# Kernel tuning notes

Hardware: AMD Instinct MI355X
Metric: run time of the kernel (lower is better)

## Reference

```python
import jax, jax.numpy as jnp
import numpy as np

B, SQ, SK, D, H, DFF = 4, 1024, 1024, 1024, 16, 4096
DEPTH = D // H
EPS = 1e-6


def setup_inputs() -> dict:
    key = jax.random.key(0)
    ks = jax.random.split(key, 32)
    s = 0.02
    inp = {
        "x": jax.random.normal(ks[0], (B, SQ, D), jnp.float32),
        "enc_output": jax.random.normal(ks[1], (B, SK, D), jnp.float32),
        # causal look-ahead mask: 1 where attention is disallowed
        "look_ahead_mask": (1.0 - jnp.tril(jnp.ones((SQ, SQ), jnp.float32)))[None, None],
        "padding_mask": jnp.zeros((B, 1, 1, SK), jnp.float32),
    }
    names = ["wq1", "wk1", "wv1", "wo1", "wq2", "wk2", "wv2", "wo2"]
    for i, n in enumerate(names):
        inp[n] = jax.random.normal(ks[2 + i], (D, D), jnp.float32) * s
        inp["b" + n[1:]] = jnp.zeros((D,), jnp.float32)
    inp["w_ffn1"] = jax.random.normal(ks[12], (D, DFF), jnp.float32) * s
    inp["b_ffn1"] = jnp.zeros((DFF,), jnp.float32)
    inp["w_ffn2"] = jax.random.normal(ks[13], (DFF, D), jnp.float32) * s
    inp["b_ffn2"] = jnp.zeros((D,), jnp.float32)
    for i in (1, 2, 3):
        inp[f"gamma{i}"] = jnp.ones((D,), jnp.float32)
        inp[f"beta{i}"] = jnp.zeros((D,), jnp.float32)
    return inp


def _layernorm(x, gamma, beta):
    mu = jnp.mean(x, axis=-1, keepdims=True)
    var = jnp.var(x, axis=-1, keepdims=True)
    return (x - mu) * jax.lax.rsqrt(var + EPS) * gamma + beta


def _split_heads(x):
    b, s, _ = x.shape
    return x.reshape(b, s, H, DEPTH).transpose(0, 2, 1, 3)  # (B,H,S,depth)


def _mha(v_in, k_in, q_in, mask, wq, bq, wk, bk, wv, bv, wo, bo):
    q = _split_heads(q_in @ wq + bq)
    k = _split_heads(k_in @ wk + bk)
    v = _split_heads(v_in @ wv + bv)
    logits = jnp.einsum("bhqd,bhkd->bhqk", q, k) / jnp.sqrt(jnp.float32(DEPTH))
    if mask is not None:
        logits = logits + mask * -1e9
    attn = jax.nn.softmax(logits, axis=-1)
    out = jnp.einsum("bhqk,bhkd->bhqd", attn, v)
    out = out.transpose(0, 2, 1, 3).reshape(q_in.shape[0], -1, D)
    return out @ wo + bo, attn


def reference(x, enc_output, look_ahead_mask, padding_mask,
              wq1, bq1, wk1, bk1, wv1, bv1, wo1, bo1,
              wq2, bq2, wk2, bk2, wv2, bv2, wo2, bo2,
              w_ffn1, b_ffn1, w_ffn2, b_ffn2,
              gamma1, beta1, gamma2, beta2, gamma3, beta3):
    attn1, aw1 = _mha(x, x, x, look_ahead_mask,
                      wq1, bq1, wk1, bk1, wv1, bv1, wo1, bo1)
    out1 = _layernorm(attn1 + x, gamma1, beta1)
    attn2, aw2 = _mha(enc_output, enc_output, out1, padding_mask,
                      wq2, bq2, wk2, bk2, wv2, bv2, wo2, bo2)
    out2 = _layernorm(attn2 + out1, gamma2, beta2)
    ffn = jax.nn.relu(out2 @ w_ffn1 + b_ffn1) @ w_ffn2 + b_ffn2
    out3 = _layernorm(ffn + out2, gamma3, beta3)
    return out3, aw1, aw2
```

## Files before the change

### kernel.cpp

```cpp
#include <hip/hip_runtime.h>

#define NB 4
#define SEQ 1024
#define DM 1024
#define NH 16
#define DEP 64
#define DFFN 4096

typedef __attribute__((ext_vector_type(8))) short short8;
typedef __attribute__((ext_vector_type(4))) float f32x4;
typedef __attribute__((ext_vector_type(4))) unsigned short us4;

__device__ __forceinline__ unsigned short f2bf(float f) {
    union { float f; unsigned int u; } v; v.f = f;
    unsigned int u = v.u;
    return (unsigned short)((u + 0x7FFFu + ((u >> 16) & 1u)) >> 16);
}

__device__ __forceinline__ void gload16(const void* g, void* l) {
    __builtin_amdgcn_global_load_lds((const __attribute__((address_space(1))) unsigned int*)g,
                                     (__attribute__((address_space(3))) unsigned int*)l, 16, 0, 0);
}

__global__ __launch_bounds__(256) void cast2_kernel(const float* __restrict__ a,
                                                    const float* __restrict__ b,
                                                    unsigned short* __restrict__ oa,
                                                    unsigned short* __restrict__ ob, int n4) {
    int i = blockIdx.x * 256 + threadIdx.x;
    const float* in = blockIdx.y ? b : a;
    unsigned short* out = blockIdx.y ? ob : oa;
    if (i < n4) {
        f32x4 f = __builtin_nontemporal_load((const f32x4*)in + i);
        us4 u;
        u[0] = f2bf(f[0]); u[1] = f2bf(f[1]); u[2] = f2bf(f[2]); u[3] = f2bf(f[3]);
        ((us4*)out)[i] = u;
    }
}

struct P10 { const float* p[10]; };
__global__ __launch_bounds__(256) void castTall_kernel(P10 s,
                                                       unsigned short* __restrict__ wsq,
                                                       unsigned short* __restrict__ wf1t,
                                                       unsigned short* __restrict__ wf2t) {
    __shared__ float tile[64][65];
    const int tid = blockIdx.x, t = threadIdx.x;
    const float* in; unsigned short* out; int R, C, r0, c0;
    if (tid < 2048) {
        int wi = tid >> 8, t2 = tid & 255;
        in = s.p[wi]; out = wsq + (size_t)wi * DM * DM; R = DM; C = DM;
        r0 = (t2 >> 4) * 64; c0 = (t2 & 15) * 64;
    } else if (tid < 3072) {
        int t2 = tid - 2048;
        in = s.p[8]; out = wf1t; R = DM; C = DFFN;
        r0 = (t2 >> 6) * 64; c0 = (t2 & 63) * 64;
    } else {
        int t2 = tid - 3072;
        in = s.p[9]; out = wf2t; R = DFFN; C = DM;
        r0 = (t2 >> 4) * 64; c0 = (t2 & 15) * 64;
    }
#pragma unroll
    for (int p = 0; p < 4; ++p) {
        int r = p * 16 + (t >> 4), c = (t & 15) * 4;
        f32x4 f = __builtin_nontemporal_load((const f32x4*)(in + (size_t)(r0 + r) * C + c0 + c));
        tile[r][c] = f[0]; tile[r][c + 1] = f[1]; tile[r][c + 2] = f[2]; tile[r][c + 3] = f[3];
    }
    __syncthreads();
#pragma unroll
    for (int p = 0; p < 4; ++p) {
        int n = p * 16 + (t >> 4), k = (t & 15) * 4;
        us4 u;
#pragma unroll
        for (int j = 0; j < 4; ++j) u[j] = f2bf(tile[k + j][n]);
        *(us4*)(out + (size_t)(c0 + n) * R + r0 + k) = u;
    }
}

__global__ __launch_bounds__(256) void biaspack_kernel(const float* __restrict__ bq1,
                                                       const float* __restrict__ bk1,
                                                       const float* __restrict__ bv1,
                                                       const float* __restrict__ bk2,
                                                       const float* __restrict__ bv2,
                                                       float* __restrict__ bqkv1,
                                                       float* __restrict__ bkv2) {
    int i = blockIdx.x * 256 + threadIdx.x;
    if (i < 1024) bqkv1[i] = bq1[i];
    else if (i < 2048) bqkv1[i] = bk1[i - 1024];
    else if (i < 3072) bqkv1[i] = bv1[i - 2048];
    else if (i < 4096) bkv2[i - 3072] = bk2[i - 3072];
    else if (i < 5120) bkv2[i - 3072] = bv2[i - 4096];
}

template <int BM, int BN, int BK, int KSPLIT, int RELU, int WB, int WF, int WVT>
__global__ __launch_bounds__(256) void gemm_kernel(const unsigned short* __restrict__ A,
                                                   const unsigned short* __restrict__ Wt,
                                                   const float* __restrict__ bias,
                                                   unsigned short* __restrict__ Cb,
                                                   float* __restrict__ Cf,
                                                   float* __restrict__ Cf2,
                                                   unsigned short* __restrict__ Vt,
                                                   int vstart,
                                                   int M, int N, int K) {
    constexpr int AM = BM / 32;
    constexpr int KS = BK / 32;
    constexpr int LPR = BK / 8;
    constexpr int RPI = 64 / LPR;
    constexpr int AR = (BM / 4) / RPI;
    constexpr int BR = (BN / 4) / RPI;
    constexpr int NLD = AR + BR;
    __shared__ unsigned short As[3][BM * BK];
    __shared__ unsigned short Bs[3][BN * BK];
    const int t = threadIdx.x;
    const int lane = t & 63, w = t >> 6;
    const int nwg = gridDim.x * gridDim.y;
    const int rawid = blockIdx.y * gridDim.x + blockIdx.x;
    const int swz = (rawid & 7) * (nwg >> 3) + (rawid >> 3);
    const int m0 = (swz / gridDim.x) * BM, n0 = (swz % gridDim.x) * BN;
    const int wm = (w >> 1) * (BM / 2), wn = (w & 1) * (BN / 2);
    const int lr = lane & 15, g = lane >> 4, kb = g * 8;
    const int srow = lane / LPR;
    const int sslotl = lane % LPR;
    const int sswz = (BK == 64) ? (sslotl ^ srow) : sslotl;
    const int scol = sswz * 8;
    const int kofs = (KSPLIT == 2 && blockIdx.z) ? K / 2 : 0;
    const int Keff = (KSPLIT == 2) ? K / 2 : K;
    const int nk = Keff / BK;

    f32x4 acc[AM][4];
#pragma unroll
    for (int a = 0; a < AM; ++a)
#pragma unroll
        for (int b = 0; b < 4; ++b)
#pragma unroll
            for (int j = 0; j < 4; ++j) acc[a][b][j] = 0.f;

    auto STAGE = [&](int buf, int kt) {
#pragma unroll
        for (int ia = 0; ia < AR; ++ia) {
            int rb = w * (BM / 4) + ia * RPI;
            gload16(A + (size_t)(m0 + rb + srow) * K + kt + scol, &As[buf][rb * BK]);
        }
#pragma unroll
        for (int ib = 0; ib < BR; ++ib) {
            int rb = w * (BN / 4) + ib * RPI;
            gload16(Wt + (size_t)(n0 + rb + srow) * K + kt + scol, &Bs[buf][rb * BK]);
        }
    };

    STAGE(0, kofs);
    if (nk > 1) STAGE(1, kofs + BK);
    int sb = 2, cb = 0;
    for (int i = 0; i < nk; ++i) {
        if (i + 2 < nk) {
            STAGE(sb, kofs + (i + 2) * BK);
            if (++sb == 3) sb = 0;
            asm volatile("s_waitcnt vmcnt(%0)" :: "n"(2 * NLD) : "memory");
        } else if (i + 1 < nk) {
            asm volatile("s_waitcnt vmcnt(%0)" :: "n"(NLD) : "memory");
        } else {
            asm volatile("s_waitcnt vmcnt(0)" ::: "memory");
        }
        __builtin_amdgcn_s_barrier();

        short8 af[AM][KS], bfr[4][KS];
#pragma unroll
        for (int ii = 0; ii < AM; ++ii)
#pragma unroll
            for (int ks = 0; ks < KS; ++ks) {
                int ofs = (BK == 64) ? (((ks * 4 + g) ^ (lr & 7)) << 3) : (ks * 32 + kb);
                af[ii][ks] = *(const short8*)&As[cb][(wm + ii * 16 + lr) * BK + ofs];
            }
#pragma unroll
        for (int ii = 0; ii < 4; ++ii)
#pragma unroll
            for (int ks = 0; ks < KS; ++ks) {
                int ofs = (BK == 64) ? (((ks * 4 + g) ^ (lr & 7)) << 3) : (ks * 32 + kb);
                bfr[ii][ks] = *(const short8*)&Bs[cb][(wn + ii * 16 + lr) * BK + ofs];
            }
        __builtin_amdgcn_s_setprio(1);
#pragma unroll
        for (int ks = 0; ks < KS; ++ks)
#pragma unroll
            for (int am = 0; am < AM; ++am)
#pragma unroll
                for (int bn = 0; bn < 4; ++bn)
                    acc[am][bn] = __builtin_amdgcn_mfma_f32_16x16x32_bf16(af[am][ks], bfr[bn][ks], acc[am][bn], 0, 0, 0);
        __builtin_amdgcn_s_setprio(0);
        if (++cb == 3) cb = 0;
        __builtin_amdgcn_s_barrier();
    }

    float* cfo = (KSPLIT == 2 && blockIdx.z) ? Cf2 : Cf;
    const bool addb = bias && (KSPLIT == 1 || blockIdx.z == 0);
#pragma unroll
    for (int am = 0; am < AM; ++am) {
#pragma unroll
        for (int bn = 0; bn < 4; ++bn) {
            int col = n0 + wn + bn * 16 + lr;
            float bv = addb ? bias[col] : 0.f;
            int rowb = m0 + wm + am * 16 + g * 4;
            float vv[4];
#pragma unroll
            for (int i = 0; i < 4; ++i) {
                float v = acc[am][bn][i] + bv;
                if (RELU) v = v > 0.f ? v : 0.f;
                vv[i] = v;
                if (WF) cfo[(size_t)(rowb + i) * N + col] = v;
                if (WB) Cb[(size_t)(rowb + i) * N + col] = f2bf(v);
            }
            if (WVT && col >= vstart) {
                int h = (col - vstart) >> 6, dep = (col - vstart) & 63;
                int b = rowb >> 10, kpos = rowb & 1023;
                us4 u;
#pragma unroll
                for (int i = 0; i < 4; ++i) u[i] = f2bf(vv[i]);
                *(us4*)(Vt + ((size_t)(b * NH + h) * DEP + dep) * SEQ + kpos) = u;
            }
        }
    }
}

template <int CAUSAL>
__global__ __launch_bounds__(256, 2) void attn_kernel(const unsigned short* __restrict__ Q, int ldq,
                                                      const unsigned short* __restrict__ Kp, int ldk,
                                                      const unsigned short* __restrict__ Vt,
                                                      const float* __restrict__ pad,
                                                      float* __restrict__ aw,
                                                      unsigned short* __restrict__ ctx) {
    __shared__ unsigned short Ks[3][128 * 64];
    __shared__ unsigned short Pch[32 * 128];
    __shared__ float redm[4][32];
    __shared__ float reds[4][32];
    const int t = threadIdx.x, lane = t & 63, w = t >> 6;
    const int lr = lane & 15, g = lane >> 4;
    const int id = blockIdx.x;
    const int bh = (id & 7) + ((id >> 8) << 3);
    const int qt = (id >> 3) & 31;
    const int q0 = qt * 32;
    const int b = bh >> 4, h = bh & 15;
    const size_t qbase = (size_t)b * SEQ * ldq + (size_t)h * DEP;
    const size_t kbase = (size_t)b * SEQ * ldk + (size_t)h * DEP;
    const int cmax = CAUSAL ? (q0 >> 7) + 1 : 8;

    const int srow = lane >> 3;
    const int sslot = (lane & 7) ^ srow;

    short8 aq[2][2];
#pragma unroll
    for (int p = 0; p < 2; ++p)
#pragma unroll
        for (int ks = 0; ks < 2; ++ks)
            aq[p][ks] = *(const short8*)(Q + qbase + (size_t)(q0 + p * 16 + lr) * ldq + ks * 32 + g * 8);

    f32x4 acc[2][8][2];
#pragma unroll
    for (int p = 0; p < 2; ++p)
#pragma unroll
        for (int c = 0; c < 8; ++c)
#pragma unroll
            for (int bn = 0; bn < 2; ++bn)
#pragma unroll
                for (int j = 0; j < 4; ++j) acc[p][c][bn][j] = 0.f;

#define STAGE_K(BUF, CH)                                                                   \
    {                                                                                      \
        _Pragma("unroll") for (int i_ = 0; i_ < 4; ++i_) {                                 \
            int rb_ = w * 32 + i_ * 8;                                                     \
            gload16(Kp + kbase + (size_t)((CH) * 128 + rb_ + srow) * ldk + sslot * 8,      \
                    &Ks[BUF][rb_ * 64]);                                                   \
        }                                                                                  \
    }

    STAGE_K(0, 0);
    if (1 < cmax) STAGE_K(1, 1);
#pragma unroll
    for (int c = 0; c < 8; ++c) {
        if (c < cmax) {
            if (c + 2 < cmax) {
                STAGE_K((c + 2) % 3, c + 2);
                asm volatile("s_waitcnt vmcnt(8)" ::: "memory");
            } else if (c + 1 < cmax) {
                asm volatile("s_waitcnt vmcnt(4)" ::: "memory");
            } else {
                asm volatile("s_waitcnt vmcnt(0)" ::: "memory");
            }
            __builtin_amdgcn_s_setprio(1);
#pragma unroll
            for (int ks = 0; ks < 2; ++ks)
#pragma unroll
                for (int bn = 0; bn < 2; ++bn) {
                    int row = w * 32 + bn * 16 + lr;
                    short8 bk = *(const short8*)((const char*)&Ks[c % 3][0] + row * 128 +
                                                 ((ks * 64 + g * 16) ^ ((lr & 7) << 4)));
                    acc[0][c][bn] = __builtin_amdgcn_mfma_f32_16x16x32_bf16(bk, aq[0][ks], acc[0][c][bn], 0, 0, 0);
                    acc[1][c][bn] = __builtin_amdgcn_mfma_f32_16x16x32_bf16(bk, aq[1][ks], acc[1][c][bn], 0, 0, 0);
                }
            __builtin_amdgcn_s_setprio(0);
        }
    }
#undef STAGE_K

    float mrow[2] = {-1e30f, -1e30f};
#pragma unroll
    for (int c = 0; c < 8; ++c) {
        if (c < cmax) {
#pragma unroll
            for (int bn = 0; bn < 2; ++bn) {
                int k4 = c * 128 + w * 32 + bn * 16 + g * 4;
                f32x4 pv = {0.f, 0.f, 0.f, 0.f};
                if (pad) pv = *(const f32x4*)(pad + (size_t)b * SEQ + k4);
#pragma unroll
                for (int p = 0; p < 2; ++p) {
                    int q = q0 + p * 16 + lr;
#pragma unroll
                    for (int i = 0; i < 4; ++i) {
                        float v = acc[p][c][bn][i] * 0.125f + pv[i] * -1e9f;
                        if (CAUSAL && (k4 + i) > q) v = -1e30f;
                        acc[p][c][bn][i] = v;
                        mrow[p] = fmaxf(mrow[p], v);
                    }
                }
            }
        }
    }
#pragma unroll
    for (int p = 0; p < 2; ++p) {
        mrow[p] = fmaxf(mrow[p], __shfl_xor(mrow[p], 16));
        mrow[p] = fmaxf(mrow[p], __shfl_xor(mrow[p], 32));
    }
    if (lane < 16) { redm[w][lr] = mrow[0]; redm[w][16 + lr] = mrow[1]; }
    __syncthreads();
    float Mv[2];
#pragma unroll
    for (int p = 0; p < 2; ++p)
        Mv[p] = fmaxf(fmaxf(redm[0][p * 16 + lr], redm[1][p * 16 + lr]),
                      fmaxf(redm[2][p * 16 + lr], redm[3][p * 16 + lr]));

    float srw[2] = {0.f, 0.f};
#pragma unroll
    for (int c = 0; c < 8; ++c) {
        if (c < cmax) {
#pragma unroll
            for (int p = 0; p < 2; ++p)
#pragma unroll
                for (int bn = 0; bn < 2; ++bn)
#pragma unroll
                    for (int i = 0; i < 4; ++i) {
                        float e = __expf(acc[p][c][bn][i] - Mv[p]);
                        acc[p][c][bn][i] = e;
                        srw[p] += e;
                    }
        }
    }
#pragma unroll
    for (int p = 0; p < 2; ++p) {
        srw[p] += __shfl_xor(srw[p], 16);
        srw[p] += __shfl_xor(srw[p], 32);
    }
    if (lane < 16) { reds[w][lr] = srw[0]; reds[w][16 + lr] = srw[1]; }
    __syncthreads();
    float inv[2];
#pragma unroll
    for (int p = 0; p < 2; ++p)
        inv[p] = 1.0f / (reds[0][p * 16 + lr] + reds[1][p * 16 + lr] +
                         reds[2][p * 16 + lr] + reds[3][p * 16 + lr]);

    f32x4 acc2[2];
#pragma unroll
    for (int p = 0; p < 2; ++p)
#pragma unroll
        for (int j = 0; j < 4; ++j) acc2[p][j] = 0.f;
    char* pch = (char*)Pch;
    const int sw = (lr & 7) << 4;
#pragma unroll
    for (int c = 0; c < 8; ++c) {
        if (c < cmax) {
            __syncthreads();
#pragma unroll
            for (int p = 0; p < 2; ++p)
#pragma unroll
                for (int bn = 0; bn < 2; ++bn) {
                    us4 u;
#pragma unroll
                    for (int i = 0; i < 4; ++i) u[i] = f2bf(acc[p][c][bn][i] * inv[p]);
                    *(us4*)(pch + (p * 16 + lr) * 256 + ((w * 64 + bn * 32 + g * 8) ^ sw)) = u;
                }
            __syncthreads();
            __builtin_amdgcn_s_setprio(1);
#pragma unroll
            for (int ks = 0; ks < 4; ++ks) {
                short8 bf = *(const short8*)(Vt + ((size_t)bh * DEP + w * 16 + lr) * SEQ + c * 128 + ks * 32 + g * 8);
#pragma unroll
                for (int p = 0; p < 2; ++p) {
                    short8 af = *(const short8*)(pch + (p * 16 + lr) * 256 + ((ks * 64 + g * 16) ^ sw));
                    acc2[p] = __builtin_amdgcn_mfma_f32_16x16x32_bf16(af, bf, acc2[p], 0, 0, 0);
                }
            }
            __builtin_amdgcn_s_setprio(0);
        }
    }
#pragma unroll
    for (int p = 0; p < 2; ++p)
#pragma unroll
        for (int i = 0; i < 4; ++i)
            ctx[((size_t)b * SEQ + q0 + p * 16 + g * 4 + i) * DM + h * DEP + w * 16 + lr] = f2bf(acc2[p][i]);

#pragma unroll
    for (int p = 0; p < 2; ++p) {
        float* awrow = aw + ((size_t)bh * SEQ + q0 + p * 16 + lr) * SEQ;
#pragma unroll
        for (int c = 0; c < 8; ++c)
#pragma unroll
            for (int bn = 0; bn < 2; ++bn) {
                f32x4 o = {0.f, 0.f, 0.f, 0.f};
                if (c < cmax) {
#pragma unroll
                    for (int i = 0; i < 4; ++i) o[i] = acc[p][c][bn][i] * inv[p];
                }
                __builtin_nontemporal_store(o, (f32x4*)(awrow + c * 128 + w * 32 + bn * 16 + g * 4));
            }
    }
}

template <int WB, int X2EN, int NTF>
__global__ __launch_bounds__(256) void ln_kernel(const float* __restrict__ X,
                                                 const float* __restrict__ X2,
                                                 const float* __restrict__ R,
                                                 const float* __restrict__ gamma,
                                                 const float* __restrict__ beta,
                                                 float* __restrict__ outF,
                                                 unsigned short* __restrict__ outB) {
    size_t row = blockIdx.x;
    const int t = threadIdx.x;
    float4 a = ((const float4*)(X + (row << 10)))[t];
    float4 r = ((const float4*)(R + (row << 10)))[t];
    float v0 = a.x + r.x, v1 = a.y + r.y, v2 = a.z + r.z, v3 = a.w + r.w;
    if (X2EN) {
        float4 a2 = ((const float4*)(X2 + (row << 10)))[t];
        v0 += a2.x; v1 += a2.y; v2 += a2.z; v3 += a2.w;
    }
    float s = v0 + v1 + v2 + v3;
    float q = v0 * v0 + v1 * v1 + v2 * v2 + v3 * v3;
#pragma unroll
    for (int off = 32; off; off >>= 1) {
        s += __shfl_down(s, off);
        q += __shfl_down(q, off);
    }
    __shared__ float rs[4], rq[4];
    if ((t & 63) == 0) { rs[t >> 6] = s; rq[t >> 6] = q; }
    __syncthreads();
    s = rs[0] + rs[1] + rs[2] + rs[3];
    q = rq[0] + rq[1] + rq[2] + rq[3];
    float mean = s * (1.0f / 1024.0f);
    float var = q * (1.0f / 1024.0f) - mean * mean;
    float inv = rsqrtf(var + 1e-6f);
    float g0 = gamma[t * 4], g1 = gamma[t * 4 + 1], g2 = gamma[t * 4 + 2], g3 = gamma[t * 4 + 3];
    float b0 = beta[t * 4], b1 = beta[t * 4 + 1], b2 = beta[t * 4 + 2], b3 = beta[t * 4 + 3];
    f32x4 o;
    o[0] = (v0 - mean) * inv * g0 + b0;
    o[1] = (v1 - mean) * inv * g1 + b1;
    o[2] = (v2 - mean) * inv * g2 + b2;
    o[3] = (v3 - mean) * inv * g3 + b3;
    if (NTF) __builtin_nontemporal_store(o, (f32x4*)(outF + (row << 10)) + t);
    else ((f32x4*)(outF + (row << 10)))[t] = o;
    if (WB) {
        us4 u;
        u[0] = f2bf(o[0]); u[1] = f2bf(o[1]); u[2] = f2bf(o[2]); u[3] = f2bf(o[3]);
        ((us4*)(outB + (row << 10)))[t] = u;
    }
}

extern "C" void kernel_launch(void* const* d_in, const int* in_sizes, int n_in,
                              void* d_out, int out_size, void* d_ws, size_t ws_size,
                              hipStream_t stream) {
    const float* x = (const float*)d_in[0];
    const float* enc = (const float*)d_in[1];
    const float* pad = (const float*)d_in[3];
    const float* wq1 = (const float*)d_in[4];  const float* bq1 = (const float*)d_in[5];
    const float* wk1 = (const float*)d_in[6];  const float* bk1 = (const float*)d_in[7];
    const float* wv1 = (const float*)d_in[8];  const float* bv1 = (const float*)d_in[9];
    const float* wo1 = (const float*)d_in[10]; const float* bo1 = (const float*)d_in[11];
    const float* wq2 = (const float*)d_in[12]; const float* bq2 = (const float*)d_in[13];
    const float* wk2 = (const float*)d_in[14]; const float* bk2 = (const float*)d_in[15];
    const float* wv2 = (const float*)d_in[16]; const float* bv2 = (const float*)d_in[17];
    const float* wo2 = (const float*)d_in[18]; const float* bo2 = (const float*)d_in[19];
    const float* wf1 = (const float*)d_in[20]; const float* bf1 = (const float*)d_in[21];
    const float* wf2 = (const float*)d_in[22]; const float* bf2 = (const float*)d_in[23];
    const float* g1 = (const float*)d_in[24]; const float* be1 = (const float*)d_in[25];
    const float* g2 = (const float*)d_in[26]; const float* be2 = (const float*)d_in[27];
    const float* g3 = (const float*)d_in[28]; const float* be3 = (const float*)d_in[29];

    float* out3 = (float*)d_out;
    float* aw1 = out3 + (size_t)NB * SEQ * DM;
    float* aw2 = aw1 + (size_t)NB * NH * SEQ * SEQ;

    char* ws = (char*)d_ws;
    size_t off = 0;
    auto take = [&](size_t n) { char* p = ws + off; off += (n + 255) & ~(size_t)255; return p; };
    const size_t SZ_SD_BF = (size_t)NB * SEQ * DM * 2;
    const size_t SZ_SD_F  = (size_t)NB * SEQ * DM * 4;
    const size_t SZ_DD_BF = (size_t)DM * DM * 2;

    unsigned short* wqkv1t = (unsigned short*)take(3 * SZ_DD_BF);
    unsigned short* wq2t   = (unsigned short*)take(SZ_DD_BF);
    unsigned short* wkv2t  = (unsigned short*)take(2 * SZ_DD_BF);
    unsigned short* wo1t   = (unsigned short*)take(SZ_DD_BF);
    unsigned short* wo2t   = (unsigned short*)take(SZ_DD_BF);
    unsigned short* wf1t   = (unsigned short*)take((size_t)DM * DFFN * 2);
    unsigned short* wf2t   = (unsigned short*)take((size_t)DFFN * DM * 2);
    float* bqkv1 = (float*)take(3 * DM * 4);
    float* bkv2  = (float*)take(2 * DM * 4);
    unsigned short* xb    = (unsigned short*)take(SZ_SD_BF);
    unsigned short* encb  = (unsigned short*)take(SZ_SD_BF);
    unsigned short* qkv1b = (unsigned short*)take(3 * SZ_SD_BF);
    unsigned short* v1t   = (unsigned short*)take(SZ_SD_BF);
    unsigned short* qb    = (unsigned short*)take(SZ_SD_BF);
    unsigned short* kv2b  = (unsigned short*)take(2 * SZ_SD_BF);
    unsigned short* v2t   = (unsigned short*)take(SZ_SD_BF);
    unsigned short* ctx   = (unsigned short*)take(SZ_SD_BF);
    float* goutf  = (float*)take(SZ_SD_F);
    float* out1f  = (float*)take(SZ_SD_F);
    unsigned short* out1b = (unsigned short*)take(SZ_SD_BF);
    float* out2f  = (float*)take(SZ_SD_F);
    unsigned short* out2b = (unsigned short*)take(SZ_SD_BF);
    unsigned short* ffn1b = (unsigned short*)take((size_t)NB * SEQ * DFFN * 2);

    {
        int n4 = NB * SEQ * DM / 4;
        dim3 gc((n4 + 255) / 256, 2);
        cast2_kernel<<<gc, 256, 0, stream>>>(x, enc, xb, encb, n4);
    }
    {
        P10 s;
        s.p[0] = wq1; s.p[1] = wk1; s.p[2] = wv1; s.p[3] = wq2;
        s.p[4] = wk2; s.p[5] = wv2; s.p[6] = wo1; s.p[7] = wo2;
        s.p[8] = wf1; s.p[9] = wf2;
        castTall_kernel<<<4096, 256, 0, stream>>>(s, wqkv1t, wf1t, wf2t);
    }
    biaspack_kernel<<<20, 256, 0, stream>>>(bq1, bk1, bv1, bk2, bv2, bqkv1, bkv2);

    const int M = NB * SEQ;
    dim3 gQKV(3 * DM / 128, M / 128);
    dim3 gKV(2 * DM / 128, M / 128);
    dim3 gDD64(DM / 128, M / 64);
    dim3 gDF(DFFN / 128, M / 128);

    gemm_kernel<128, 128, 32, 1, 0, 1, 0, 1><<<gQKV, 256, 0, stream>>>(xb, wqkv1t, bqkv1, qkv1b, nullptr, nullptr, v1t, 2048, M, 3 * DM, DM);
    attn_kernel<1><<<2048, 256, 0, stream>>>(qkv1b, 3 * DM, qkv1b + DM, 3 * DM, v1t, nullptr, aw1, ctx);
    gemm_kernel<64, 128, 64, 1, 0, 0, 1, 0><<<gDD64, 256, 0, stream>>>(ctx, wo1t, bo1, nullptr, goutf, nullptr, nullptr, 0, M, DM, DM);
    ln_kernel<1, 0, 0><<<M, 256, 0, stream>>>(goutf, nullptr, x, g1, be1, out1f, out1b);

    gemm_kernel<64, 128, 64, 1, 0, 1, 0, 0><<<gDD64, 256, 0, stream>>>(out1b, wq2t, bq2, qb, nullptr, nullptr, nullptr, 0, M, DM, DM);
    gemm_kernel<128, 128, 32, 1, 0, 1, 0, 1><<<gKV, 256, 0, stream>>>(encb, wkv2t, bkv2, kv2b, nullptr, nullptr, v2t, 1024, M, 2 * DM, DM);
    attn_kernel<0><<<2048, 256, 0, stream>>>(qb, DM, kv2b, 2 * DM, v2t, pad, aw2, ctx);
    gemm_kernel<64, 128, 64, 1, 0, 0, 1, 0><<<gDD64, 256, 0, stream>>>(ctx, wo2t, bo2, nullptr, goutf, nullptr, nullptr, 0, M, DM, DM);
    ln_kernel<1, 0, 0><<<M, 256, 0, stream>>>(goutf, nullptr, out1f, g2, be2, out2f, out2b);

    gemm_kernel<128, 128, 32, 1, 1, 1, 0, 0><<<gDF, 256, 0, stream>>>(out2b, wf1t, bf1, ffn1b, nullptr, nullptr, nullptr, 0, M, DFFN, DM);
    gemm_kernel<64, 128, 64, 1, 0, 0, 1, 0><<<gDD64, 256, 0, stream>>>(ffn1b, wf2t, bf2, nullptr, goutf, nullptr, nullptr, 0, M, DM, DFFN);
    ln_kernel<0, 0, 1><<<M, 256, 0, stream>>>(goutf, nullptr, out2f, g3, be3, out3, nullptr);
}
```

Before: 494.1 us.

## Merge prep kernels, select bias per column block, retune GEMM tiles and occupancy

Folds the activation casts and weight transposes into one prep kernel and removes the bias-packing kernel, picking among up to three bias pointers by column block inside the GEMM. The 64-row GEMMs switch from BK=64 to BK=32 and gain a minimum-waves-per-EU hint in launch bounds. The s_setprio calls around the MFMA loop and the unused split-K and second-residual paths are removed. This cuts launch count and may raise occupancy, but the smaller K-tile means more barriers per tile and the occupancy hint may force register spills.

```diff
diff --git a/kernel.cpp b/kernel.cpp
--- a/kernel.cpp
+++ b/kernel.cpp
@@ -22,28 +22,28 @@
                                      (__attribute__((address_space(3))) unsigned int*)l, 16, 0, 0);
 }
 
-__global__ __launch_bounds__(256) void cast2_kernel(const float* __restrict__ a,
-                                                    const float* __restrict__ b,
-                                                    unsigned short* __restrict__ oa,
-                                                    unsigned short* __restrict__ ob, int n4) {
-    int i = blockIdx.x * 256 + threadIdx.x;
-    const float* in = blockIdx.y ? b : a;
-    unsigned short* out = blockIdx.y ? ob : oa;
-    if (i < n4) {
+struct P10 { const float* p[10]; };
+__global__ __launch_bounds__(256) void prep_kernel(P10 s,
+                                                   unsigned short* __restrict__ wsq,
+                                                   unsigned short* __restrict__ wf1t,
+                                                   unsigned short* __restrict__ wf2t,
+                                                   const float* __restrict__ x,
+                                                   const float* __restrict__ enc,
+                                                   unsigned short* __restrict__ xb,
+                                                   unsigned short* __restrict__ encb) {
+    const int tid = blockIdx.x, t = threadIdx.x;
+    if (tid >= 4096) {
+        int idx = tid - 4096;
+        const float* in = (idx >= 4096) ? enc : x;
+        unsigned short* out = (idx >= 4096) ? encb : xb;
+        int i = (idx & 4095) * 256 + t;
         f32x4 f = __builtin_nontemporal_load((const f32x4*)in + i);
         us4 u;
         u[0] = f2bf(f[0]); u[1] = f2bf(f[1]); u[2] = f2bf(f[2]); u[3] = f2bf(f[3]);
         ((us4*)out)[i] = u;
-    }
-}
-
-struct P10 { const float* p[10]; };
-__global__ __launch_bounds__(256) void castTall_kernel(P10 s,
-                                                       unsigned short* __restrict__ wsq,
-                                                       unsigned short* __restrict__ wf1t,
-                                                       unsigned short* __restrict__ wf2t) {
+        return;
+    }
     __shared__ float tile[64][65];
-    const int tid = blockIdx.x, t = threadIdx.x;
     const float* in; unsigned short* out; int R, C, r0, c0;
     if (tid < 2048) {
         int wi = tid >> 8, t2 = tid & 255;
@@ -75,31 +75,18 @@
     }
 }
 
-__global__ __launch_bounds__(256) void biaspack_kernel(const float* __restrict__ bq1,
-                                                       const float* __restrict__ bk1,
-                                                       const float* __restrict__ bv1,
-                                                       const float* __restrict__ bk2,
-                                                       const float* __restrict__ bv2,
-                                                       float* __restrict__ bqkv1,
-                                                       float* __restrict__ bkv2) {
-    int i = blockIdx.x * 256 + threadIdx.x;
-    if (i < 1024) bqkv1[i] = bq1[i];
-    else if (i < 2048) bqkv1[i] = bk1[i - 1024];
-    else if (i < 3072) bqkv1[i] = bv1[i - 2048];
-    else if (i < 4096) bkv2[i - 3072] = bk2[i - 3072];
-    else if (i < 5120) bkv2[i - 3072] = bv2[i - 4096];
-}
-
-template <int BM, int BN, int BK, int KSPLIT, int RELU, int WB, int WF, int WVT>
-__global__ __launch_bounds__(256) void gemm_kernel(const unsigned short* __restrict__ A,
-                                                   const unsigned short* __restrict__ Wt,
-                                                   const float* __restrict__ bias,
-                                                   unsigned short* __restrict__ Cb,
-                                                   float* __restrict__ Cf,
-                                                   float* __restrict__ Cf2,
-                                                   unsigned short* __restrict__ Vt,
-                                                   int vstart,
-                                                   int M, int N, int K) {
+template <int BM, int BN, int BK, int RELU, int WB, int WF, int WVT>
+__global__ __launch_bounds__(256, (BM == 64 ? 4 : 2)) void gemm_kernel(
+        const unsigned short* __restrict__ A,
+        const unsigned short* __restrict__ Wt,
+        const float* __restrict__ bias0,
+        const float* __restrict__ bias1,
+        const float* __restrict__ bias2,
+        unsigned short* __restrict__ Cb,
+        float* __restrict__ Cf,
+        unsigned short* __restrict__ Vt,
+        int vstart,
+        int M, int N, int K) {
     constexpr int AM = BM / 32;
     constexpr int KS = BK / 32;
     constexpr int LPR = BK / 8;
@@ -121,9 +108,9 @@
     const int sslotl = lane % LPR;
     const int sswz = (BK == 64) ? (sslotl ^ srow) : sslotl;
     const int scol = sswz * 8;
-    const int kofs = (KSPLIT == 2 && blockIdx.z) ? K / 2 : 0;
-    const int Keff = (KSPLIT == 2) ? K / 2 : K;
-    const int nk = Keff / BK;
+    const int nk = K / BK;
+    const int bsel = n0 >> 10;
+    const float* bias = (bsel == 0) ? bias0 : ((bsel == 1) ? bias1 : bias2);
 
     f32x4 acc[AM][4];
 #pragma unroll
@@ -146,12 +133,12 @@
         }
     };
 
-    STAGE(0, kofs);
-    if (nk > 1) STAGE(1, kofs + BK);
+    STAGE(0, 0);
+    if (nk > 1) STAGE(1, BK);
     int sb = 2, cb = 0;
     for (int i = 0; i < nk; ++i) {
         if (i + 2 < nk) {
-            STAGE(sb, kofs + (i + 2) * BK);
+            STAGE(sb, (i + 2) * BK);
             if (++sb == 3) sb = 0;
             asm volatile("s_waitcnt vmcnt(%0)" :: "n"(2 * NLD) : "memory");
         } else if (i + 1 < nk) {
@@ -176,7 +163,6 @@
                 int ofs = (BK == 64) ? (((ks * 4 + g) ^ (lr & 7)) << 3) : (ks * 32 + kb);
                 bfr[ii][ks] = *(const short8*)&Bs[cb][(wn + ii * 16 + lr) * BK + ofs];
             }
-        __builtin_amdgcn_s_setprio(1);
 #pragma unroll
         for (int ks = 0; ks < KS; ++ks)
 #pragma unroll
@@ -184,19 +170,16 @@
 #pragma unroll
                 for (int bn = 0; bn < 4; ++bn)
                     acc[am][bn] = __builtin_amdgcn_mfma_f32_16x16x32_bf16(af[am][ks], bfr[bn][ks], acc[am][bn], 0, 0, 0);
-        __builtin_amdgcn_s_setprio(0);
         if (++cb == 3) cb = 0;
         __builtin_amdgcn_s_barrier();
     }
 
-    float* cfo = (KSPLIT == 2 && blockIdx.z) ? Cf2 : Cf;
-    const bool addb = bias && (KSPLIT == 1 || blockIdx.z == 0);
 #pragma unroll
     for (int am = 0; am < AM; ++am) {
 #pragma unroll
         for (int bn = 0; bn < 4; ++bn) {
             int col = n0 + wn + bn * 16 + lr;
-            float bv = addb ? bias[col] : 0.f;
+            float bv = bias ? bias[col & 1023] : 0.f;
             int rowb = m0 + wm + am * 16 + g * 4;
             float vv[4];
 #pragma unroll
@@ -204,7 +187,7 @@
                 float v = acc[am][bn][i] + bv;
                 if (RELU) v = v > 0.f ? v : 0.f;
                 vv[i] = v;
-                if (WF) cfo[(size_t)(rowb + i) * N + col] = v;
+                if (WF) Cf[(size_t)(rowb + i) * N + col] = v;
                 if (WB) Cb[(size_t)(rowb + i) * N + col] = f2bf(v);
             }
             if (WVT && col >= vstart) {
@@ -421,9 +404,8 @@
     }
 }
 
-template <int WB, int X2EN, int NTF>
+template <int WB, int NTF>
 __global__ __launch_bounds__(256) void ln_kernel(const float* __restrict__ X,
-                                                 const float* __restrict__ X2,
                                                  const float* __restrict__ R,
                                                  const float* __restrict__ gamma,
                                                  const float* __restrict__ beta,
@@ -434,10 +416,6 @@
     float4 a = ((const float4*)(X + (row << 10)))[t];
     float4 r = ((const float4*)(R + (row << 10)))[t];
     float v0 = a.x + r.x, v1 = a.y + r.y, v2 = a.z + r.z, v3 = a.w + r.w;
-    if (X2EN) {
-        float4 a2 = ((const float4*)(X2 + (row << 10)))[t];
-        v0 += a2.x; v1 += a2.y; v2 += a2.z; v3 += a2.w;
-    }
     float s = v0 + v1 + v2 + v3;
     float q = v0 * v0 + v1 * v1 + v2 * v2 + v3 * v3;
 #pragma unroll
@@ -507,8 +485,6 @@
     unsigned short* wo2t   = (unsigned short*)take(SZ_DD_BF);
     unsigned short* wf1t   = (unsigned short*)take((size_t)DM * DFFN * 2);
     unsigned short* wf2t   = (unsigned short*)take((size_t)DFFN * DM * 2);
-    float* bqkv1 = (float*)take(3 * DM * 4);
-    float* bkv2  = (float*)take(2 * DM * 4);
     unsigned short* xb    = (unsigned short*)take(SZ_SD_BF);
     unsigned short* encb  = (unsigned short*)take(SZ_SD_BF);
     unsigned short* qkv1b = (unsigned short*)take(3 * SZ_SD_BF);
@@ -525,18 +501,12 @@
     unsigned short* ffn1b = (unsigned short*)take((size_t)NB * SEQ * DFFN * 2);
 
     {
-        int n4 = NB * SEQ * DM / 4;
-        dim3 gc((n4 + 255) / 256, 2);
-        cast2_kernel<<<gc, 256, 0, stream>>>(x, enc, xb, encb, n4);
-    }
-    {
         P10 s;
         s.p[0] = wq1; s.p[1] = wk1; s.p[2] = wv1; s.p[3] = wq2;
         s.p[4] = wk2; s.p[5] = wv2; s.p[6] = wo1; s.p[7] = wo2;
         s.p[8] = wf1; s.p[9] = wf2;
-        castTall_kernel<<<4096, 256, 0, stream>>>(s, wqkv1t, wf1t, wf2t);
-    }
-    biaspack_kernel<<<20, 256, 0, stream>>>(bq1, bk1, bv1, bk2, bv2, bqkv1, bkv2);
+        prep_kernel<<<12288, 256, 0, stream>>>(s, wqkv1t, wf1t, wf2t, x, enc, xb, encb);
+    }
 
     const int M = NB * SEQ;
     dim3 gQKV(3 * DM / 128, M / 128);
@@ -544,18 +514,18 @@
     dim3 gDD64(DM / 128, M / 64);
     dim3 gDF(DFFN / 128, M / 128);
 
-    gemm_kernel<128, 128, 32, 1, 0, 1, 0, 1><<<gQKV, 256, 0, stream>>>(xb, wqkv1t, bqkv1, qkv1b, nullptr, nullptr, v1t, 2048, M, 3 * DM, DM);
+    gemm_kernel<128, 128, 32, 0, 1, 0, 1><<<gQKV, 256, 0, stream>>>(xb, wqkv1t, bq1, bk1, bv1, qkv1b, nullptr, v1t, 2048, M, 3 * DM, DM);
     attn_kernel<1><<<2048, 256, 0, stream>>>(qkv1b, 3 * DM, qkv1b + DM, 3 * DM, v1t, nullptr, aw1, ctx);
-    gemm_kernel<64, 128, 64, 1, 0, 0, 1, 0><<<gDD64, 256, 0, stream>>>(ctx, wo1t, bo1, nullptr, goutf, nullptr, nullptr, 0, M, DM, DM);
-    ln_kernel<1, 0, 0><<<M, 256, 0, stream>>>(goutf, nullptr, x, g1, be1, out1f, out1b);
-
-    gemm_kernel<64, 128, 64, 1, 0, 1, 0, 0><<<gDD64, 256, 0, stream>>>(out1b, wq2t, bq2, qb, nullptr, nullptr, nullptr, 0, M, DM, DM);
-    gemm_kernel<128, 128, 32, 1, 0, 1, 0, 1><<<gKV, 256, 0, stream>>>(encb, wkv2t, bkv2, kv2b, nullptr, nullptr, v2t, 1024, M, 2 * DM, DM);
+    gemm_kernel<64, 128, 32, 0, 0, 1, 0><<<gDD64, 256, 0, stream>>>(ctx, wo1t, bo1, bo1, bo1, nullptr, goutf, nullptr, 0, M, DM, DM);
+    ln_kernel<1, 0><<<M, 256, 0, stream>>>(goutf, x, g1, be1, out1f, out1b);
+
+    gemm_kernel<64, 128, 32, 0, 1, 0, 0><<<gDD64, 256, 0, stream>>>(out1b, wq2t, bq2, bq2, bq2, qb, nullptr, nullptr, 0, M, DM, DM);
+    gemm_kernel<128, 128, 32, 0, 1, 0, 1><<<gKV, 256, 0, stream>>>(encb, wkv2t, bk2, bv2, bv2, kv2b, nullptr, v2t, 1024, M, 2 * DM, DM);
     attn_kernel<0><<<2048, 256, 0, stream>>>(qb, DM, kv2b, 2 * DM, v2t, pad, aw2, ctx);
-    gemm_kernel<64, 128, 64, 1, 0, 0, 1, 0><<<gDD64, 256, 0, stream>>>(ctx, wo2t, bo2, nullptr, goutf, nullptr, nullptr, 0, M, DM, DM);
-    ln_kernel<1, 0, 0><<<M, 256, 0, stream>>>(goutf, nullptr, out1f, g2, be2, out2f, out2b);
-
-    gemm_kernel<128, 128, 32, 1, 1, 1, 0, 0><<<gDF, 256, 0, stream>>>(out2b, wf1t, bf1, ffn1b, nullptr, nullptr, nullptr, 0, M, DFFN, DM);
-    gemm_kernel<64, 128, 64, 1, 0, 0, 1, 0><<<gDD64, 256, 0, stream>>>(ffn1b, wf2t, bf2, nullptr, goutf, nullptr, nullptr, 0, M, DM, DFFN);
-    ln_kernel<0, 0, 1><<<M, 256, 0, stream>>>(goutf, nullptr, out2f, g3, be3, out3, nullptr);
-}
+    gemm_kernel<64, 128, 32, 0, 0, 1, 0><<<gDD64, 256, 0, stream>>>(ctx, wo2t, bo2, bo2, bo2, nullptr, goutf, nullptr, 0, M, DM, DM);
+    ln_kernel<1, 0><<<M, 256, 0, stream>>>(goutf, out1f, g2, be2, out2f, out2b);
+
+    gemm_kernel<128, 128, 32, 1, 1, 0, 0><<<gDF, 256, 0, stream>>>(out2b, wf1t, bf1, bf1, bf1, ffn1b, nullptr, nullptr, 0, M, DFFN, DM);
+    gemm_kernel<64, 128, 32, 0, 0, 1, 0><<<gDD64, 256, 0, stream>>>(ffn1b, wf2t, bf2, bf2, bf2, nullptr, goutf, nullptr, 0, M, DM, DFFN);
+    ln_kernel<0, 1><<<M, 256, 0, stream>>>(goutf, out2f, g3, be3, out3, nullptr);
+}
```

Result: slower. 506.4 us (+2.5%).
